# Kernel optimization log

Hardware: AMD Instinct MI355X
Metric: run time of the kernel (lower is better)

Reference implementation:

```python
import jax, jax.numpy as jnp
import numpy as np
import math

EMB = 1024
H = 8          # num_heads
HD = EMB // H // 2  # head_dim = 64
LAMBDA_INIT = 0.8
B, N = 2, 2048


def setup_inputs() -> dict:
    key = jax.random.key(0)
    ks = jax.random.split(key, 16)
    s = 1.0 / math.sqrt(EMB)
    d = {
        'q': jax.random.normal(ks[0], (B, N, EMB), jnp.float32),
        'k': jax.random.normal(ks[1], (B, N, EMB), jnp.float32),
        'v': jax.random.normal(ks[2], (B, N, EMB), jnp.float32),
        'Wq': jax.random.uniform(ks[3], (EMB, EMB), jnp.float32, -s, s),
        'bq': jax.random.uniform(ks[4], (EMB,), jnp.float32, -s, s),
        'Wk': jax.random.uniform(ks[5], (EMB, EMB), jnp.float32, -s, s),
        'bk': jax.random.uniform(ks[6], (EMB,), jnp.float32, -s, s),
        'Wv': jax.random.uniform(ks[7], (EMB, EMB), jnp.float32, -s, s),
        'bv': jax.random.uniform(ks[8], (EMB,), jnp.float32, -s, s),
        'Wo': jax.random.uniform(ks[9], (EMB, EMB), jnp.float32, -s, s),
        'bo': jax.random.uniform(ks[10], (EMB,), jnp.float32, -s, s),
        'lambda_q1': 0.1 * jax.random.normal(ks[11], (HD,), jnp.float32),
        'lambda_k1': 0.1 * jax.random.normal(ks[12], (HD,), jnp.float32),
        'lambda_q2': 0.1 * jax.random.normal(ks[13], (HD,), jnp.float32),
        'lambda_k2': 0.1 * jax.random.normal(ks[14], (HD,), jnp.float32),
    }
    return d


def reference(q, k, v, Wq, bq, Wk, bk, Wv, bv, Wo, bo,
              lambda_q1, lambda_k1, lambda_q2, lambda_k2):
    b, n, _ = q.shape
    # projections (torch Linear: x @ W.T + b)
    qp = q @ Wq.T + bq            # [b, n, EMB]
    kp = k @ Wk.T + bk
    vp = v @ Wv.T + bv
    # split into 2*H sub-heads of width HD for q/k; H heads of width 2*HD for v
    qh = qp.reshape(b, n, 2 * H, HD).transpose(0, 2, 1, 3)   # [b, 2H, n, HD]
    kh = kp.reshape(b, n, 2 * H, HD).transpose(0, 2, 1, 3)   # [b, 2H, n, HD]
    vh = vp.reshape(b, n, H, 2 * HD).transpose(0, 2, 1, 3)   # [b, H, n, 2HD]
    scale = 1.0 / math.sqrt(HD)
    attn = jnp.einsum('bhqd,bhkd->bhqk', qh, kh) * scale      # [b, 2H, n, n]
    attn = jax.nn.softmax(attn, axis=-1)
    lam1 = jnp.exp(jnp.sum(lambda_q1 * lambda_k1))
    lam2 = jnp.exp(jnp.sum(lambda_q2 * lambda_k2))
    lam = lam1 - lam2 + LAMBDA_INIT
    attn = attn.reshape(b, H, 2, n, n)
    diff = attn[:, :, 0] - lam * attn[:, :, 1]                # [b, H, n, n]
    out = jnp.einsum('bhqk,bhkd->bhqd', diff, vh)             # [b, H, n, 2HD]
    out = out.transpose(0, 2, 1, 3).reshape(b, n, H * 2 * HD)
    return out @ Wo.T + bo
```

## Files before the change

### kernel.cpp

```cpp
#include <hip/hip_runtime.h>
#include <stdint.h>


typedef __attribute__((ext_vector_type(8))) __bf16 bf16x8;
typedef __attribute__((ext_vector_type(4))) __bf16 bf16x4;
typedef __attribute__((ext_vector_type(4))) float f32x4;
typedef __attribute__((ext_vector_type(16))) float f32x16;
typedef __attribute__((ext_vector_type(8))) unsigned short u16x8;
typedef __attribute__((ext_vector_type(4))) unsigned short u16x4;
typedef __attribute__((ext_vector_type(4))) unsigned int u32x4;
typedef unsigned short u16;
typedef unsigned int u32;

#define EMB 1024
#define NSEQ 2048
#define NBATCH 2
#define NHEAD 8
#define MROWS (NBATCH*NSEQ)
#define QSCALE 0.18033688011112042f

__device__ __forceinline__ u16x4 pk4(float a, float b, float c, float d){
  bf16x4 h; h[0]=(__bf16)a; h[1]=(__bf16)b; h[2]=(__bf16)c; h[3]=(__bf16)d;
  return __builtin_bit_cast(u16x4, h);
}
__device__ __forceinline__ u16 bf1(float f){
  __bf16 h = (__bf16)f; return __builtin_bit_cast(unsigned short, h);
}
__device__ __forceinline__ u32 cvtpk(float lo, float hi){
  u32 r; asm("v_cvt_pk_bf16_f32 %0, %1, %2" : "=v"(r) : "v"(lo), "v"(hi)); return r;
}

__device__ __forceinline__ bf16x8 ld8(const u16* p){
  return __builtin_bit_cast(bf16x8, *(const u16x8*)p);
}

__device__ __forceinline__ void glds16(const u16* g, u16* l){
  __builtin_amdgcn_global_load_lds(
      (const __attribute__((address_space(1))) u32*)g,
      (__attribute__((address_space(3))) u32*)l, 16, 0, 0);
}

__global__ void cvt_k(const float* __restrict__ q, const float* __restrict__ k,
                      const float* __restrict__ v, const float* __restrict__ Wq,
                      const float* __restrict__ Wk, const float* __restrict__ Wv,
                      const float* __restrict__ Wo,
                      const float* __restrict__ lq1, const float* __restrict__ lk1,
                      const float* __restrict__ lq2, const float* __restrict__ lk2,
                      u16* qb, u16* kb, u16* vb, u16* Wqb, u16* Wkb, u16* Wvb, u16* Wob,
                      float* lam)
{
  if (blockIdx.x == 0 && threadIdx.x < 64){
    int l = threadIdx.x;
    float p1 = lq1[l]*lk1[l];
    float p2 = lq2[l]*lk2[l];
    #pragma unroll
    for (int m=1; m<64; m<<=1){ p1 += __shfl_xor(p1, m, 64); p2 += __shfl_xor(p2, m, 64); }
    if (l==0) lam[0] = __expf(p1) - __expf(p2) + 0.8f;
  }
  const int NQ4 = (NBATCH*NSEQ*EMB)/4;
  const int NW4 = (EMB*EMB)/4;
  const int total = 3*NQ4 + 4*NW4;
  for (int i = blockIdx.x*blockDim.x + threadIdx.x; i < total; i += gridDim.x*blockDim.x){
    const float* src; u16* dst; int off;
    if (i < 3*NQ4){
      int t = i / NQ4; off = i - t*NQ4;
      src = t==0 ? q : (t==1 ? k : v);
      dst = t==0 ? qb : (t==1 ? kb : vb);
    } else {
      int j = i - 3*NQ4;
      int t = j / NW4; off = j - t*NW4;
      src = t==0 ? Wq : (t==1 ? Wk : (t==2 ? Wv : Wo));
      dst = t==0 ? Wqb : (t==1 ? Wkb : (t==2 ? Wvb : Wob));
    }
    f32x4 f = *((const f32x4*)src + off);
    *((u16x4*)dst + off) = pk4(f[0], f[1], f[2], f[3]);
  }
}

__device__ __forceinline__ void gemm_core(
    const u16* __restrict__ A, const u16* __restrict__ W, const float* __restrict__ bias,
    u16* __restrict__ Ybf, u16* __restrict__ Yvt, int mode,
    float oscale, u16* As, u16* Bs)
{
  const int tid = threadIdx.x, w = tid >> 6, l = tid & 63;
  const int l15 = l & 15, lg = l >> 4;
  const int m0 = blockIdx.y * 128, n0 = blockIdx.x * 128;
  const int wr = w >> 1, wc = w & 1;
  const int srow = w*16 + (l >> 2);
  const int skel = (l & 3) * 8;

  f32x4 acc[4][4] = {};

  for (int kt = 0; kt < EMB/32; ++kt){
    const int kb = kt*32 + skel;
    glds16(A + (size_t)(m0 + srow)*EMB + kb,      As + w*512);
    glds16(A + (size_t)(m0 + 64 + srow)*EMB + kb, As + 2048 + w*512);
    glds16(W + (size_t)(n0 + srow)*EMB + kb,      Bs + w*512);
    glds16(W + (size_t)(n0 + 64 + srow)*EMB + kb, Bs + 2048 + w*512);
    __syncthreads();

    bf16x8 af[4], bfr[4];
    #pragma unroll
    for (int mi=0; mi<4; ++mi) af[mi]  = ld8(As + (wr*64 + mi*16 + l15)*32 + lg*8);
    #pragma unroll
    for (int ni=0; ni<4; ++ni) bfr[ni] = ld8(Bs + (wc*64 + ni*16 + l15)*32 + lg*8);
    #pragma unroll
    for (int mi=0; mi<4; ++mi)
      #pragma unroll
      for (int ni=0; ni<4; ++ni)
        acc[mi][ni] = __builtin_amdgcn_mfma_f32_16x16x32_bf16(af[mi], bfr[ni], acc[mi][ni], 0,0,0);
    __syncthreads();
  }

  #pragma unroll
  for (int mi=0; mi<4; ++mi){
    const int mr = m0 + wr*64 + mi*16 + lg*4;
    #pragma unroll
    for (int ni=0; ni<4; ++ni){
      const int nc = n0 + wc*64 + ni*16 + l15;
      const float bvs = bias[nc]*oscale;
      if (mode == 0){
        #pragma unroll
        for (int i=0;i<4;++i) Ybf[(size_t)(mr+i)*EMB + nc] = bf1(fmaf(acc[mi][ni][i], oscale, bvs));
      } else {
        const int h = nc >> 7, vd = nc & 127, bb = mr >> 11, t = mr & 2047;
        u16x4 pkv = pk4(acc[mi][ni][0]+bvs, acc[mi][ni][1]+bvs,
                        acc[mi][ni][2]+bvs, acc[mi][ni][3]+bvs);
        *(u16x4*)(Yvt + ((size_t)((bb*NHEAD + h)*128 + vd))*NSEQ + t) = pkv;
      }
    }
  }
}

__global__ __launch_bounds__(256) void gemm_qkv(
    const u16* qb, const u16* kb, const u16* vb,
    const u16* Wqb, const u16* Wkb, const u16* Wvb,
    const float* bq, const float* bk, const float* bv,
    u16* Qp, u16* Kp, u16* Vt)
{
  __shared__ __align__(16) u16 As[4096], Bs[4096];
  const int z = blockIdx.z;
  const u16* A = z==0 ? qb : (z==1 ? kb : vb);
  const u16* W = z==0 ? Wqb : (z==1 ? Wkb : Wvb);
  const float* bias = z==0 ? bq : (z==1 ? bk : bv);
  if (z == 0)      gemm_core(A, W, bias, Qp, nullptr, 0, QSCALE, As, Bs);
  else if (z == 1) gemm_core(A, W, bias, Kp, nullptr, 0, 1.0f, As, Bs);
  else             gemm_core(A, W, bias, nullptr, Vt, 1, 1.0f, As, Bs);
}

__global__ __launch_bounds__(256) void gemm_out_k(
    const u16* __restrict__ Xc, const u16* __restrict__ Wob,
    const float* __restrict__ bo, float* __restrict__ out)
{
  __shared__ __align__(16) u16 As[2048], Bs[4096];
  const int tid = threadIdx.x, w = tid >> 6, l = tid & 63;
  const int l15 = l & 15, lg = l >> 4;
  const int m0 = blockIdx.y * 64, n0 = blockIdx.x * 128;
  const int wr = w >> 1, wc = w & 1;
  const int srow = w*16 + (l >> 2);
  const int skel = (l & 3) * 8;

  f32x4 acc[2][4] = {};

  for (int kt = 0; kt < EMB/32; ++kt){
    const int kb = kt*32 + skel;
    glds16(Xc  + (size_t)(m0 + srow)*EMB + kb,      As + w*512);
    glds16(Wob + (size_t)(n0 + srow)*EMB + kb,      Bs + w*512);
    glds16(Wob + (size_t)(n0 + 64 + srow)*EMB + kb, Bs + 2048 + w*512);
    __syncthreads();

    bf16x8 af[2], bfr[4];
    #pragma unroll
    for (int mi=0; mi<2; ++mi) af[mi]  = ld8(As + (wr*32 + mi*16 + l15)*32 + lg*8);
    #pragma unroll
    for (int ni=0; ni<4; ++ni) bfr[ni] = ld8(Bs + (wc*64 + ni*16 + l15)*32 + lg*8);
    #pragma unroll
    for (int mi=0; mi<2; ++mi)
      #pragma unroll
      for (int ni=0; ni<4; ++ni)
        acc[mi][ni] = __builtin_amdgcn_mfma_f32_16x16x32_bf16(af[mi], bfr[ni], acc[mi][ni], 0,0,0);
    __syncthreads();
  }

  #pragma unroll
  for (int mi=0; mi<2; ++mi){
    const int mr = m0 + wr*32 + mi*16 + lg*4;
    #pragma unroll
    for (int ni=0; ni<4; ++ni){
      const int nc = n0 + wc*64 + ni*16 + l15;
      const float bv = bo[nc];
      #pragma unroll
      for (int i=0;i<4;++i) out[(size_t)(mr+i)*EMB + nc] = acc[mi][ni][i] + bv;
    }
  }
}

__global__ __launch_bounds__(512, 4) void attn_k(
    const u16* __restrict__ Qp, const u16* __restrict__ Kp,
    const u16* __restrict__ Vt, const float* __restrict__ lamp,
    u16* __restrict__ Xc)
{
  __shared__ __align__(16) char shm[66560];
  u16* ldsK = (u16*)shm;
  u16* ldsV = (u16*)(shm + 32768);

  const int tid = threadIdx.x, w = tid >> 6, l = tid & 63;
  const int l31 = l & 31, hl = l >> 5;
  const int qg = w & 1, s = (w >> 1) & 1, g = w >> 2;
  const int wg = w & 3;
  int bid = blockIdx.x;
  bid = (bid & 7)*64 + (bid >> 3);
  const int qt = bid & 31, bh = bid >> 5;
  const int b = bh >> 3, h = bh & 7;
  const int q0 = qt*64 + qg*32;

  const u16* Kg = Kp + ((size_t)b*NSEQ)*EMB + h*128;
  const u16* Vg = Vt + ((size_t)((b*NHEAD + h)*128))*NSEQ;

  const u16* qbase = Qp + (size_t)(b*NSEQ + q0 + l31)*EMB + (2*h + s)*64;
  bf16x8 qa[4];
  #pragma unroll
  for (int ks=0; ks<4; ++ks) qa[ks] = ld8(qbase + ks*16 + hl*8);

  f32x16 acc[4] = {};
  float l_run = 0.f;

  auto STAGE = [&](int buf, int t){
    const u16* kg = Kg + (size_t)t*32*EMB;
    u16* kd = ldsK + (g*2 + buf)*4096;
    #pragma unroll
    for (int j=0;j<2;++j){
      int row = wg*8 + j*4 + (l >> 4);
      glds16(kg + (size_t)row*EMB + (((l&15) ^ (row&15))*8), kd + (wg*8 + j*4)*128);
    }
    const u16* vg = Vg + t*32;
    u16* vd2 = ldsV + (g*2 + buf)*4096;
    #pragma unroll
    for (int j=0;j<2;++j){
      int row = wg*32 + j*16 + (l >> 2);
      glds16(vg + (size_t)row*NSEQ + (((l&3) ^ ((row>>1)&3))*8), vd2 + (wg*32 + j*16)*32);
    }
  };

  auto BODY = [&](const u16* Kb, const u16* Vb){
    f32x16 st = {};
    __builtin_amdgcn_s_setprio(1);
    #pragma unroll
    for (int ks=0; ks<4; ++ks){
      int c = s*8 + ks*2 + hl;
      bf16x8 kf = ld8(Kb + l31*128 + ((c ^ (l31&15))*8));
      st = __builtin_amdgcn_mfma_f32_32x32x16_bf16(kf, qa[ks], st, 0,0,0);
    }
    __builtin_amdgcn_s_setprio(0);

    float p[16];
    #pragma unroll
    for (int r=0; r<16; ++r) p[r] = exp2f(st[r]);
    float s0 = (p[0]+p[1]) + (p[2]+p[3]);
    float s1 = (p[4]+p[5]) + (p[6]+p[7]);
    float s2 = (p[8]+p[9]) + (p[10]+p[11]);
    float s3 = (p[12]+p[13]) + (p[14]+p[15]);
    float ssum = (s0+s1) + (s2+s3);
    ssum += __shfl_xor(ssum, 32, 64);
    l_run += ssum;

    bf16x8 pa[2];
    #pragma unroll
    for (int kb=0; kb<2; ++kb){
      u32 w0 = cvtpk(p[8*kb+0], p[8*kb+1]);
      u32 w1 = cvtpk(p[8*kb+2], p[8*kb+3]);
      u32 w2 = cvtpk(p[8*kb+4], p[8*kb+5]);
      u32 w3 = cvtpk(p[8*kb+6], p[8*kb+7]);
      asm volatile("v_permlane32_swap_b32 %0, %1" : "+v"(w0), "+v"(w2));
      asm volatile("v_permlane32_swap_b32 %0, %1" : "+v"(w1), "+v"(w3));
      u32x4 t4; t4[0]=w0; t4[1]=w1; t4[2]=w2; t4[3]=w3;
      pa[kb] = __builtin_bit_cast(bf16x8, t4);
    }

    __builtin_amdgcn_s_setprio(1);
    #pragma unroll
    for (int kb=0; kb<2; ++kb)
      #pragma unroll
      for (int v=0; v<4; ++v){
        int row = v*32 + l31;
        int kc = kb*2 + hl;
        bf16x8 vf = ld8(Vb + row*32 + ((kc ^ ((row>>1)&3))*8));
        acc[v] = __builtin_amdgcn_mfma_f32_32x32x16_bf16(vf, pa[kb], acc[v], 0,0,0);
      }
    __builtin_amdgcn_s_setprio(0);
  };

  const u16* Kb0 = ldsK + (g*2 + 0)*4096;  const u16* Vb0 = ldsV + (g*2 + 0)*4096;
  const u16* Kb1 = ldsK + (g*2 + 1)*4096;  const u16* Vb1 = ldsV + (g*2 + 1)*4096;

  STAGE(0, g);
  __syncthreads();

  for (int jj = 0; jj < 16; ++jj){
    STAGE(1, 2*(2*jj+1) + g);
    BODY(Kb0, Vb0);
    __syncthreads();
    if (jj < 15) STAGE(0, 2*(2*jj+2) + g);
    BODY(Kb1, Vb1);
    __syncthreads();
  }

  float* pool = (float*)shm;
  float* lsh  = (float*)(shm + 65536);
  const int slot = qg*2 + s;

  if (g == 1){
    #pragma unroll
    for (int v=0; v<4; ++v)
      #pragma unroll
      for (int rr=0; rr<4; ++rr){
        f32x4 t4; t4[0]=acc[v][rr*4+0]; t4[1]=acc[v][rr*4+1];
        t4[2]=acc[v][rr*4+2]; t4[3]=acc[v][rr*4+3];
        *(f32x4*)(pool + (((slot*4 + v)*4 + rr)*64 + l)*4) = t4;
      }
    if (hl == 0) lsh[slot*32 + l31] = l_run;
  }
  __syncthreads();
  float L = 1.f;
  if (g == 0){
    L = l_run + lsh[slot*32 + l31];
    #pragma unroll
    for (int v=0; v<4; ++v)
      #pragma unroll
      for (int rr=0; rr<4; ++rr){
        f32x4 c = *(f32x4*)(pool + (((slot*4 + v)*4 + rr)*64 + l)*4);
        #pragma unroll
        for (int e=0; e<4; ++e) acc[v][rr*4+e] += c[e];
      }
  }
  __syncthreads();
  if (g == 0 && s == 1){
    const float f = lamp[0] / L;
    #pragma unroll
    for (int v=0; v<4; ++v)
      #pragma unroll
      for (int rr=0; rr<4; ++rr){
        f32x4 t4; t4[0]=acc[v][rr*4+0]*f; t4[1]=acc[v][rr*4+1]*f;
        t4[2]=acc[v][rr*4+2]*f; t4[3]=acc[v][rr*4+3]*f;
        *(f32x4*)(pool + (((qg*4 + v)*4 + rr)*64 + l)*4) = t4;
      }
  }
  __syncthreads();
  if (g == 0 && s == 0){
    const float i0 = 1.f / L;
    #pragma unroll
    for (int v=0; v<4; ++v)
      #pragma unroll
      for (int rr=0; rr<4; ++rr){
        f32x4 c = *(f32x4*)(pool + (((qg*4 + v)*4 + rr)*64 + l)*4);
        u16x4 o = pk4(acc[v][rr*4+0]*i0 - c[0], acc[v][rr*4+1]*i0 - c[1],
                      acc[v][rr*4+2]*i0 - c[2], acc[v][rr*4+3]*i0 - c[3]);
        const int col = v*32 + rr*8 + hl*4;
        *(u16x4*)(Xc + (size_t)(b*NSEQ + q0 + l31)*EMB + h*128 + col) = o;
      }
  }
}

extern "C" void kernel_launch(void* const* d_in, const int* in_sizes, int n_in,
                              void* d_out, int out_size, void* d_ws, size_t ws_size,
                              hipStream_t stream)
{
  const float* q   = (const float*)d_in[0];
  const float* k   = (const float*)d_in[1];
  const float* v   = (const float*)d_in[2];
  const float* Wq  = (const float*)d_in[3];
  const float* bq  = (const float*)d_in[4];
  const float* Wk  = (const float*)d_in[5];
  const float* bk  = (const float*)d_in[6];
  const float* Wv  = (const float*)d_in[7];
  const float* bv  = (const float*)d_in[8];
  const float* Wo  = (const float*)d_in[9];
  const float* bo  = (const float*)d_in[10];
  const float* lq1 = (const float*)d_in[11];
  const float* lk1 = (const float*)d_in[12];
  const float* lq2 = (const float*)d_in[13];
  const float* lk2 = (const float*)d_in[14];

  const size_t NQ = (size_t)MROWS*EMB;
  const size_t NW = (size_t)EMB*EMB;
  u16* qb  = (u16*)d_ws;
  u16* kb  = qb + NQ;
  u16* vb  = kb + NQ;
  u16* Wqb = vb + NQ;
  u16* Wkb = Wqb + NW;
  u16* Wvb = Wkb + NW;
  u16* Wob = Wvb + NW;
  u16* Qp  = Wob + NW;
  u16* Kp  = Qp + NQ;
  u16* Vt  = Kp + NQ;
  u16* Xc  = Vt + NQ;
  float* lam = (float*)(Xc + NQ);

  cvt_k<<<2048, 256, 0, stream>>>(q, k, v, Wq, Wk, Wv, Wo,
                                  lq1, lk1, lq2, lk2,
                                  qb, kb, vb, Wqb, Wkb, Wvb, Wob, lam);
  gemm_qkv<<<dim3(EMB/128, MROWS/128, 3), 256, 0, stream>>>(
      qb, kb, vb, Wqb, Wkb, Wvb, bq, bk, bv, Qp, Kp, Vt);
  attn_k<<<dim3(NBATCH*NHEAD*(NSEQ/64)), 512, 0, stream>>>(Qp, Kp, Vt, lam, Xc);
  gemm_out_k<<<dim3(EMB/128, MROWS/64), 256, 0, stream>>>(Xc, Wob, bo, (float*)d_out);
}
```

Before: 149.6 us.

## Fuse fp32-to-bf16 activation conversion into QKV projection GEMM loads

```diff
diff --git a/kernel.cpp b/kernel.cpp
--- a/kernel.cpp
+++ b/kernel.cpp
@@ -26,6 +26,12 @@
 __device__ __forceinline__ u16 bf1(float f){
   __bf16 h = (__bf16)f; return __builtin_bit_cast(unsigned short, h);
 }
+__device__ __forceinline__ u16x8 pk8(f32x4 a, f32x4 b){
+  u16x8 r;
+  r[0]=bf1(a[0]); r[1]=bf1(a[1]); r[2]=bf1(a[2]); r[3]=bf1(a[3]);
+  r[4]=bf1(b[0]); r[5]=bf1(b[1]); r[6]=bf1(b[2]); r[7]=bf1(b[3]);
+  return r;
+}
 __device__ __forceinline__ u32 cvtpk(float lo, float hi){
   u32 r; asm("v_cvt_pk_bf16_f32 %0, %1, %2" : "=v"(r) : "v"(lo), "v"(hi)); return r;
 }
@@ -40,14 +46,11 @@
       (__attribute__((address_space(3))) u32*)l, 16, 0, 0);
 }
 
-__global__ void cvt_k(const float* __restrict__ q, const float* __restrict__ k,
-                      const float* __restrict__ v, const float* __restrict__ Wq,
-                      const float* __restrict__ Wk, const float* __restrict__ Wv,
-                      const float* __restrict__ Wo,
+__global__ void cvt_w(const float* __restrict__ Wq, const float* __restrict__ Wk,
+                      const float* __restrict__ Wv, const float* __restrict__ Wo,
                       const float* __restrict__ lq1, const float* __restrict__ lk1,
                       const float* __restrict__ lq2, const float* __restrict__ lk2,
-                      u16* qb, u16* kb, u16* vb, u16* Wqb, u16* Wkb, u16* Wvb, u16* Wob,
-                      float* lam)
+                      u16* Wqb, u16* Wkb, u16* Wvb, u16* Wob, float* lam)
 {
   if (blockIdx.x == 0 && threadIdx.x < 64){
     int l = threadIdx.x;
@@ -57,30 +60,21 @@
     for (int m=1; m<64; m<<=1){ p1 += __shfl_xor(p1, m, 64); p2 += __shfl_xor(p2, m, 64); }
     if (l==0) lam[0] = __expf(p1) - __expf(p2) + 0.8f;
   }
-  const int NQ4 = (NBATCH*NSEQ*EMB)/4;
   const int NW4 = (EMB*EMB)/4;
-  const int total = 3*NQ4 + 4*NW4;
+  const int total = 4*NW4;
   for (int i = blockIdx.x*blockDim.x + threadIdx.x; i < total; i += gridDim.x*blockDim.x){
-    const float* src; u16* dst; int off;
-    if (i < 3*NQ4){
-      int t = i / NQ4; off = i - t*NQ4;
-      src = t==0 ? q : (t==1 ? k : v);
-      dst = t==0 ? qb : (t==1 ? kb : vb);
-    } else {
-      int j = i - 3*NQ4;
-      int t = j / NW4; off = j - t*NW4;
-      src = t==0 ? Wq : (t==1 ? Wk : (t==2 ? Wv : Wo));
-      dst = t==0 ? Wqb : (t==1 ? Wkb : (t==2 ? Wvb : Wob));
-    }
+    int t = i / NW4, off = i - t*NW4;
+    const float* src = t==0 ? Wq : (t==1 ? Wk : (t==2 ? Wv : Wo));
+    u16* dst        = t==0 ? Wqb : (t==1 ? Wkb : (t==2 ? Wvb : Wob));
     f32x4 f = *((const f32x4*)src + off);
     *((u16x4*)dst + off) = pk4(f[0], f[1], f[2], f[3]);
   }
 }
 
-__device__ __forceinline__ void gemm_core(
-    const u16* __restrict__ A, const u16* __restrict__ W, const float* __restrict__ bias,
-    u16* __restrict__ Ybf, u16* __restrict__ Yvt, int mode,
-    float oscale, u16* As, u16* Bs)
+template<int MODE>
+__device__ __forceinline__ void gemm_core_f32A(
+    const float* __restrict__ A, const u16* __restrict__ W, const float* __restrict__ bias,
+    u16* __restrict__ Ybf, u16* __restrict__ Yvt, float oscale, u16* As, u16* Bs)
 {
   const int tid = threadIdx.x, w = tid >> 6, l = tid & 63;
   const int l15 = l & 15, lg = l >> 4;
@@ -89,14 +83,27 @@
   const int srow = w*16 + (l >> 2);
   const int skel = (l & 3) * 8;
 
+  const float* a0p = A + (size_t)(m0 + srow)*EMB;
+  const float* a1p = A + (size_t)(m0 + 64 + srow)*EMB;
+
   f32x4 acc[4][4] = {};
+
+  f32x4 r0 = *(const f32x4*)(a0p + skel);
+  f32x4 r1 = *(const f32x4*)(a0p + skel + 4);
+  f32x4 r2 = *(const f32x4*)(a1p + skel);
+  f32x4 r3 = *(const f32x4*)(a1p + skel + 4);
 
   for (int kt = 0; kt < EMB/32; ++kt){
     const int kb = kt*32 + skel;
-    glds16(A + (size_t)(m0 + srow)*EMB + kb,      As + w*512);
-    glds16(A + (size_t)(m0 + 64 + srow)*EMB + kb, As + 2048 + w*512);
     glds16(W + (size_t)(n0 + srow)*EMB + kb,      Bs + w*512);
     glds16(W + (size_t)(n0 + 64 + srow)*EMB + kb, Bs + 2048 + w*512);
+    *(u16x8*)(As + srow*32 + skel)        = pk8(r0, r1);
+    *(u16x8*)(As + 2048 + srow*32 + skel) = pk8(r2, r3);
+    const int kbn = (kt+1 < EMB/32 ? (kt+1)*32 : kt*32) + skel;
+    r0 = *(const f32x4*)(a0p + kbn);
+    r1 = *(const f32x4*)(a0p + kbn + 4);
+    r2 = *(const f32x4*)(a1p + kbn);
+    r3 = *(const f32x4*)(a1p + kbn + 4);
     __syncthreads();
 
     bf16x8 af[4], bfr[4];
@@ -119,7 +126,7 @@
     for (int ni=0; ni<4; ++ni){
       const int nc = n0 + wc*64 + ni*16 + l15;
       const float bvs = bias[nc]*oscale;
-      if (mode == 0){
+      if constexpr (MODE == 0){
         #pragma unroll
         for (int i=0;i<4;++i) Ybf[(size_t)(mr+i)*EMB + nc] = bf1(fmaf(acc[mi][ni][i], oscale, bvs));
       } else {
@@ -133,19 +140,16 @@
 }
 
 __global__ __launch_bounds__(256) void gemm_qkv(
-    const u16* qb, const u16* kb, const u16* vb,
+    const float* qf, const float* kf, const float* vf,
     const u16* Wqb, const u16* Wkb, const u16* Wvb,
     const float* bq, const float* bk, const float* bv,
     u16* Qp, u16* Kp, u16* Vt)
 {
   __shared__ __align__(16) u16 As[4096], Bs[4096];
   const int z = blockIdx.z;
-  const u16* A = z==0 ? qb : (z==1 ? kb : vb);
-  const u16* W = z==0 ? Wqb : (z==1 ? Wkb : Wvb);
-  const float* bias = z==0 ? bq : (z==1 ? bk : bv);
-  if (z == 0)      gemm_core(A, W, bias, Qp, nullptr, 0, QSCALE, As, Bs);
-  else if (z == 1) gemm_core(A, W, bias, Kp, nullptr, 0, 1.0f, As, Bs);
-  else             gemm_core(A, W, bias, nullptr, Vt, 1, 1.0f, As, Bs);
+  if (z == 0)      gemm_core_f32A<0>(qf, Wqb, bq, Qp, nullptr, QSCALE, As, Bs);
+  else if (z == 1) gemm_core_f32A<0>(kf, Wkb, bk, Kp, nullptr, 1.0f, As, Bs);
+  else             gemm_core_f32A<1>(vf, Wvb, bv, nullptr, Vt, 1.0f, As, Bs);
 }
 
 __global__ __launch_bounds__(256) void gemm_out_k(
@@ -383,10 +387,7 @@
 
   const size_t NQ = (size_t)MROWS*EMB;
   const size_t NW = (size_t)EMB*EMB;
-  u16* qb  = (u16*)d_ws;
-  u16* kb  = qb + NQ;
-  u16* vb  = kb + NQ;
-  u16* Wqb = vb + NQ;
+  u16* Wqb = (u16*)d_ws;
   u16* Wkb = Wqb + NW;
   u16* Wvb = Wkb + NW;
   u16* Wob = Wvb + NW;
@@ -396,11 +397,10 @@
   u16* Xc  = Vt + NQ;
   float* lam = (float*)(Xc + NQ);
 
-  cvt_k<<<2048, 256, 0, stream>>>(q, k, v, Wq, Wk, Wv, Wo,
-                                  lq1, lk1, lq2, lk2,
-                                  qb, kb, vb, Wqb, Wkb, Wvb, Wob, lam);
+  cvt_w<<<1024, 256, 0, stream>>>(Wq, Wk, Wv, Wo, lq1, lk1, lq2, lk2,
+                                  Wqb, Wkb, Wvb, Wob, lam);
   gemm_qkv<<<dim3(EMB/128, MROWS/128, 3), 256, 0, stream>>>(
-      qb, kb, vb, Wqb, Wkb, Wvb, bq, bk, bv, Qp, Kp, Vt);
+      q, k, v, Wqb, Wkb, Wvb, bq, bk, bv, Qp, Kp, Vt);
   attn_k<<<dim3(NBATCH*NHEAD*(NSEQ/64)), 512, 0, stream>>>(Qp, Kp, Vt, lam, Xc);
   gemm_out_k<<<dim3(EMB/128, MROWS/64), 256, 0, stream>>>(Xc, Wob, bo, (float*)d_out);
 }
```

Measured after the change: 176.6 us. +18.1%, slower.
